# Kernel tuning notes

Hardware: AMD Instinct MI355X
Metric: run time of the kernel (lower is better)

The kernel has to match this reference:

```python
import jax, jax.numpy as jnp
import numpy as np

LAM = 1e-05
NUM_POINTS = 300
THRESHOLD = 0.5


def _sobel(img):
    # img: [B, 1, H, W] -> edge magnitude [B, 1, H, W]
    kx = jnp.array([[-1., 0., 1.], [-2., 0., 2.], [-1., 0., 1.]], jnp.float32).reshape(1, 1, 3, 3)
    ky = jnp.array([[-1., -2., -1.], [0., 0., 0.], [1., 2., 1.]], jnp.float32).reshape(1, 1, 3, 3)
    dn = jax.lax.conv_dimension_numbers(img.shape, kx.shape, ('NCHW', 'OIHW', 'NCHW'))
    ex = jax.lax.conv_general_dilated(img, kx, (1, 1), ((1, 1), (1, 1)), dimension_numbers=dn)
    ey = jax.lax.conv_general_dilated(img, ky, (1, 1), ((1, 1), (1, 1)), dimension_numbers=dn)
    return jnp.sqrt(ex ** 2 + ey ** 2)


def _select_points(edge_map, key):
    # JIT-friendly analogue of nonzero + randperm[:300]: random scores on
    # above-threshold pixels, take top NUM_POINTS; invalid slots are padded
    # with a duplicate of the first valid point (zero-length MST edges, so
    # they contribute nothing to total persistence, matching fewer points).
    H, W = edge_map.shape
    flat = edge_map.reshape(-1)
    mask = flat > THRESHOLD
    scores = jnp.where(mask, jax.random.uniform(key, flat.shape), -jnp.inf)
    _, idx = jax.lax.top_k(scores, NUM_POINTS)
    valid = mask[idx]
    pts = jnp.stack([idx // W, idx % W], axis=-1).astype(jnp.float32)  # (row, col)
    pts = jnp.where(valid[:, None], pts, pts[0])
    return pts


def _mst_total_persistence(pts):
    # H0 persistence of a Vietoris-Rips complex: births are 0, deaths are the
    # MST edge lengths (Prim's algorithm via lax.scan over N-1 steps).
    # total_persistence with exponent q=2: sum(death^2).
    d2 = jnp.sum((pts[:, None, :] - pts[None, :, :]) ** 2, axis=-1)
    D = jnp.sqrt(jnp.maximum(d2, 0.0))  # [N, N]
    n = pts.shape[0]
    in_tree = jnp.zeros((n,), dtype=bool).at[0].set(True)

    def step(carry, _):
        in_tree, mind = carry
        m = jnp.where(in_tree, jnp.inf, mind)
        j = jnp.argmin(m)
        w = m[j]
        in_tree = in_tree.at[j].set(True)
        mind = jnp.minimum(mind, D[j])
        return (in_tree, mind), w

    _, deaths = jax.lax.scan(step, (in_tree, D[0]), None, length=n - 1)
    return jnp.sum(deaths ** 2)


def _topo_loss(model_output, labels):
    pred_edges = _sobel(jax.nn.sigmoid(model_output))[:, 0]  # [B, H, W]
    mask_edges = _sobel(labels)[:, 0]                         # [B, H, W]
    B = pred_edges.shape[0]
    keys = jax.random.split(jax.random.key(42), 2 * B).reshape(B, 2)

    def per_sample(pe, me, k):
        pts_p = _select_points(pe, k[0])
        pts_m = _select_points(me, k[1])
        tp_p = _mst_total_persistence(pts_p)
        tp_m = _mst_total_persistence(pts_m)
        # SummaryStatisticLoss(total_persistence): |stat(mask) - stat(pred)|
        return jnp.abs(tp_m - tp_p)

    losses = jax.vmap(per_sample)(pred_edges, mask_edges, keys)
    return LAM * jnp.sum(losses) / B


def setup_inputs() -> dict:
    key = jax.random.key(0)
    k1, k2 = jax.random.split(key)
    model_output = jax.random.normal(k1, (32, 1, 512, 512), dtype=jnp.float32)
    labels = jax.random.uniform(k2, (32, 1, 512, 512), dtype=jnp.float32)
    return {"model_output": model_output, "labels": labels}


def reference(model_output, labels):
    return _topo_loss(model_output, labels)
```

## Files before the change

kernel.cpp:

```cpp
#include <hip/hip_runtime.h>
#include <cstdint>
#include <cstddef>

#define NPIX (512 * 512)
#define NMAPS 64
#define NPTS 300
#define CAP 2048
#define SLOTS 64
#define LBUFSZ 256
#define NWORDS 4096
#define TARGET 700.0
#define MT_BITS 0xFF63C000u

__device__ __forceinline__ uint32_t umin32(uint32_t a, uint32_t b) {
  return a < b ? a : b;
}

__device__ __forceinline__ void tf2x32(uint32_t k0, uint32_t k1,
                                       uint32_t x0, uint32_t x1,
                                       uint32_t& o0, uint32_t& o1) {
  uint32_t ks2 = k0 ^ k1 ^ 0x1BD11BDAu;
#define TFR(r) { x0 += x1; x1 = (x1 << (r)) | (x1 >> (32 - (r))); x1 ^= x0; }
  x0 += k0; x1 += k1;
  TFR(13) TFR(15) TFR(26) TFR(6)
  x0 += k1; x1 += ks2 + 1u;
  TFR(17) TFR(29) TFR(16) TFR(24)
  x0 += ks2; x1 += k0 + 2u;
  TFR(13) TFR(15) TFR(26) TFR(6)
  x0 += k0; x1 += k1 + 3u;
  TFR(17) TFR(29) TFR(16) TFR(24)
  x0 += k1; x1 += ks2 + 4u;
  TFR(13) TFR(15) TFR(26) TFR(6)
  x0 += ks2; x1 += k0 + 5u;
#undef TFR
  o0 = x0; o1 = x1;
}

__device__ __forceinline__ uint32_t score23(uint32_t k0, uint32_t k1, uint32_t p) {
  uint32_t a, b;
  tf2x32(k0, k1, 0u, p, a, b);
  return (a ^ b) >> 9;
}

__device__ __forceinline__ void map_key(int m, uint32_t& k0, uint32_t& k1) {
  tf2x32(0u, 42u, 0u, (uint32_t)m, k0, k1);
}

template <int CTRL>
__device__ __forceinline__ uint32_t dpp_mov_u32(uint32_t x) {
  return (uint32_t)__builtin_amdgcn_update_dpp((int)x, (int)x, CTRL, 0xF, 0xF,
                                               false);
}

__device__ __forceinline__ uint32_t wave_min_u32_bcast(uint32_t v) {
  v = umin32(v, dpp_mov_u32<0x111>(v));
  v = umin32(v, dpp_mov_u32<0x112>(v));
  v = umin32(v, dpp_mov_u32<0x114>(v));
  v = umin32(v, dpp_mov_u32<0x118>(v));
  v = umin32(v, dpp_mov_u32<0x142>(v));
  v = umin32(v, dpp_mov_u32<0x143>(v));
  return (uint32_t)__builtin_amdgcn_readlane((int)v, 63);
}

template <bool PRED, bool YIN>
__device__ __forceinline__ void edge_body(
    const float* __restrict__ src, unsigned long long* __restrict__ bitmap,
    unsigned int* __restrict__ wcnts, unsigned long long* lbuf,
    unsigned int* lcnt, int m, int l, int cs, int seg, int wi, uint32_t k0,
    uint32_t k1) {
  const int y0 = seg * 32;
  const int X = cs * 64 + l;
  const int hcol = (l == 0) ? X - 1 : ((l == 63) ? X + 1 : -1);
  const bool hok = (unsigned)hcol < 512u;

  auto val = [&](float t) -> float {
    if constexpr (PRED) return 1.f / (1.f + __expf(-t));
    else return t;
  };
  auto ldm = [&](int row) -> float {
    if constexpr (!YIN) {
      if ((unsigned)row >= 512u) return 0.f;
    }
    return val(src[row * 512 + X]);
  };
  auto ldh = [&](int row) -> float {
    if (!hok) return 0.f;
    if constexpr (!YIN) {
      if ((unsigned)row >= 512u) return 0.f;
    }
    return val(src[row * 512 + hcol]);
  };

  float a = ldm(y0 - 1), b = ldm(y0);
  float ha = ldh(y0 - 1), hb = ldh(y0);
  unsigned int cnt = 0;

  for (int i = 0; i < 32; ++i) {
    const int y = y0 + i;
    float c = ldm(y + 1), hc = ldh(y + 1);

    float t = a + 2.f * b + c;
    float u = c - a;
    float th = ha + 2.f * hb + hc;
    float uh = hc - ha;

    float tL = __shfl_up(t, 1);   if (l == 0)  tL = th;
    float tR = __shfl_down(t, 1); if (l == 63) tR = th;
    float uL = __shfl_up(u, 1);   if (l == 0)  uL = uh;
    float uR = __shfl_down(u, 1); if (l == 63) uR = uh;

    float ex = tR - tL;
    float ey = uL + 2.f * u + uR;
    bool bit = (ex * ex + ey * ey) > 0.25f;

    unsigned long long ball = __ballot(bit);
    if (l == 0) {
      bitmap[(size_t)m * NWORDS + (size_t)y * 8 + cs] = ball;
      cnt += (unsigned int)__popcll(ball);
    }
    if (bit) {
      uint32_t p = (uint32_t)(y * 512 + X);
      uint32_t o0, o1;
      tf2x32(k0, k1, 0u, p, o0, o1);
      uint32_t x = o0 ^ o1;
      if (x >= MT_BITS) {
        unsigned int pos = atomicAdd(lcnt, 1u);
        if (pos < LBUFSZ)
          lbuf[pos] = ((unsigned long long)(x >> 9) << 32) | (uint32_t)(~p);
      }
    }
    a = b; b = c; ha = hb; hb = hc;
  }
  if (l == 0) wcnts[m * 128 + wi] = cnt;
}

__global__ __launch_bounds__(256) void edge_collect_kernel(
    const float* __restrict__ mo, const float* __restrict__ lb,
    unsigned long long* __restrict__ bitmap, unsigned int* __restrict__ wcnts,
    unsigned long long* __restrict__ cand, unsigned int* __restrict__ bcnt,
    float* __restrict__ out) {
  const int m = blockIdx.y;
  const int which = m & 1;
  const int bx = blockIdx.x;
  const float* __restrict__ src = (which ? lb : mo) + (size_t)(m >> 1) * NPIX;
  const int l = threadIdx.x & 63;
  const int wi = bx * 4 + (threadIdx.x >> 6);
  const int cs = wi & 7;
  const int seg = wi >> 3;

  if (m == 0 && bx == 0 && threadIdx.x == 0) out[0] = 0.f;

  __shared__ unsigned long long lbuf[LBUFSZ];
  __shared__ unsigned int lcnt;
  if (threadIdx.x == 0) lcnt = 0;
  __syncthreads();

  uint32_t k0, k1;
  map_key(m, k0, k1);

  const bool yin = (seg != 0) && (seg != 15);
  if (which) {
    if (yin) edge_body<false, true>(src, bitmap, wcnts, lbuf, &lcnt, m, l, cs, seg, wi, k0, k1);
    else     edge_body<false, false>(src, bitmap, wcnts, lbuf, &lcnt, m, l, cs, seg, wi, k0, k1);
  } else {
    if (yin) edge_body<true, true>(src, bitmap, wcnts, lbuf, &lcnt, m, l, cs, seg, wi, k0, k1);
    else     edge_body<true, false>(src, bitmap, wcnts, lbuf, &lcnt, m, l, cs, seg, wi, k0, k1);
  }

  __syncthreads();
  const unsigned int total = lcnt;
  const unsigned int cc = total < SLOTS ? total : SLOTS;
  for (unsigned int i = threadIdx.x; i < cc; i += 256)
    cand[(size_t)m * CAP + bx * SLOTS + i] = lbuf[i];
  if (threadIdx.x == 0) bcnt[m * 32 + bx] = total;
}

__device__ __forceinline__ void reduce_N(const unsigned int* __restrict__ wcnts,
                                         int m, int tid, unsigned int* sN) {
  if (tid < 64) {
    unsigned int v = wcnts[m * 128 + tid] + wcnts[m * 128 + 64 + tid];
#pragma unroll
    for (int off = 32; off > 0; off >>= 1) v += __shfl_xor(v, off, 64);
    if (tid == 0) *sN = v;
  }
}

__global__ __launch_bounds__(256) void select_kernel(
    const unsigned long long* __restrict__ bitmap,
    const unsigned int* __restrict__ wcnts,
    const unsigned long long* __restrict__ cand,
    const unsigned int* __restrict__ bcnt,
    uint32_t* __restrict__ pts, unsigned int* __restrict__ nsel) {
  const int m = blockIdx.x;
  const int tid = threadIdx.x;
  __shared__ unsigned long long buf[CAP];
  __shared__ unsigned int hist[256];
  __shared__ unsigned int scnt32[32];
  __shared__ unsigned int sbase[33];
  __shared__ unsigned int s_tot, s_cnt, s_b, s_rank, sN, s_ovf;

  reduce_N(wcnts, m, tid, &sN);
  if (tid < 32) scnt32[tid] = bcnt[m * 32 + tid];
  __syncthreads();
  const unsigned int N = sN;
  if (N == 0) { if (tid == 0) nsel[m] = 0; return; }
  const unsigned int need = N < NPTS ? N : NPTS;

  if (tid == 0) {
    unsigned int s = 0, ovf = 0;
    for (int i = 0; i < 32; ++i) {
      sbase[i] = s;
      unsigned int cg = scnt32[i];
      if (cg > SLOTS) ovf = 1;
      s += cg < SLOTS ? cg : SLOTS;
    }
    sbase[32] = s;
    s_ovf = ovf;
  }
  __syncthreads();

  unsigned int c;
  if (!s_ovf && sbase[32] >= need) {
    c = sbase[32];
    const int g = tid >> 3, j0 = tid & 7;
    const unsigned int cg = scnt32[g] < SLOTS ? scnt32[g] : SLOTS;
    for (unsigned int i = j0; i < cg; i += 8)
      buf[sbase[g] + i] = cand[(size_t)m * CAP + g * SLOTS + i];
    __syncthreads();
  } else {
    uint32_t k0, k1;
    map_key(m, k0, k1);
    const unsigned long long* __restrict__ wmap = bitmap + (size_t)m * NWORDS;
    unsigned int mt = 0, cnt = 0;
    double target = TARGET;
    for (int iter = 0; iter < 16; ++iter) {
      mt = ((double)N > target)
               ? (unsigned int)(8388608.0 * (1.0 - target / (double)N))
               : 0u;
      if (tid == 0) s_tot = 0;
      __syncthreads();
      unsigned int lc = 0;
      for (int w = tid; w < NWORDS; w += 256) {
        unsigned long long word = wmap[w];
        while (word) {
          int bpos = __builtin_ctzll(word);
          word &= word - 1;
          uint32_t p = ((uint32_t)w << 6) + (uint32_t)bpos;
          lc += (score23(k0, k1, p) >= mt) ? 1u : 0u;
        }
      }
      if (lc) atomicAdd(&s_tot, lc);
      __syncthreads();
      cnt = s_tot;
      __syncthreads();
      if (cnt >= need && cnt <= CAP) break;
      if (cnt < need) target *= 3.0; else target *= 0.5;
    }
    if (tid == 0) s_cnt = 0;
    __syncthreads();
    for (int w = tid; w < NWORDS; w += 256) {
      unsigned long long word = wmap[w];
      while (word) {
        int bpos = __builtin_ctzll(word);
        word &= word - 1;
        uint32_t p = ((uint32_t)w << 6) + (uint32_t)bpos;
        uint32_t sc = score23(k0, k1, p);
        if (sc >= mt) {
          unsigned int pos = atomicAdd(&s_cnt, 1u);
          if (pos < CAP)
            buf[pos] = ((unsigned long long)sc << 32) | (uint32_t)(~p);
        }
      }
    }
    __syncthreads();
    c = s_cnt < CAP ? s_cnt : CAP;
    __syncthreads();
  }

  unsigned long long T = 0ull;
  if (c > need) {
    unsigned int rank = need;
    unsigned long long prefix = 0ull;
    for (int sh = 48; sh >= 0; sh -= 8) {
      hist[tid] = 0;
      __syncthreads();
      for (unsigned int i = tid; i < c; i += 256) {
        unsigned long long k = buf[i];
        if ((k >> (sh + 8)) == (prefix >> (sh + 8)))
          atomicAdd(&hist[(unsigned int)(k >> sh) & 255u], 1u);
      }
      __syncthreads();
      if (tid < 64) {
        unsigned int h0 = hist[4 * tid], h1 = hist[4 * tid + 1];
        unsigned int h2 = hist[4 * tid + 2], h3 = hist[4 * tid + 3];
        unsigned int gsum = h0 + h1 + h2 + h3;
        unsigned int s = gsum;
#pragma unroll
        for (int off = 1; off < 64; off <<= 1) {
          unsigned int o = __shfl_down(s, off, 64);
          s += (tid + off < 64) ? o : 0u;
        }
        unsigned int above = s - gsum;
        unsigned int S3 = above, S2 = S3 + h3, S1 = S2 + h2, S0 = S1 + h1;
        if (S3 < rank && rank <= S3 + h3) { s_b = 4 * tid + 3; s_rank = rank - S3; }
        if (S2 < rank && rank <= S2 + h2) { s_b = 4 * tid + 2; s_rank = rank - S2; }
        if (S1 < rank && rank <= S1 + h1) { s_b = 4 * tid + 1; s_rank = rank - S1; }
        if (S0 < rank && rank <= S0 + h0) { s_b = 4 * tid + 0; s_rank = rank - S0; }
      }
      __syncthreads();
      prefix |= ((unsigned long long)s_b) << sh;
      rank = s_rank;
    }
    T = prefix;
  }

  if (tid == 0) s_cnt = 0;
  __syncthreads();
  for (unsigned int i = tid; i < c; i += 256) {
    unsigned long long k = buf[i];
    if (k >= T) {
      unsigned int pos = atomicAdd(&s_cnt, 1u);
      if (pos < NPTS) {
        uint32_t p = ~(uint32_t)k;
        pts[(size_t)m * NPTS + pos] = ((p >> 9) << 16) | (p & 511u);
      }
    }
  }
  __syncthreads();
  if (tid == 0) nsel[m] = s_cnt < need ? s_cnt : need;
}

__global__ __launch_bounds__(128, 1) void mst_kernel(
    const uint32_t* __restrict__ pts, const unsigned int* __restrict__ nsel,
    float* __restrict__ out) {
  const int wv = threadIdx.x >> 6;
  const int m = blockIdx.x * 2 + wv;
  const int l = threadIdx.x & 63;
  const int n = (int)nsel[m];
  __shared__ float stp[2];

  unsigned int utp = 0;
  if (n > 1) {
    uint32_t pk[5], key[5];
    int px[5], py[5];
#pragma unroll
    for (int k = 0; k < 5; ++k) {
      int id = k * 64 + l;
      pk[k] = (id < n) ? pts[(size_t)m * NPTS + id] : 0u;
    }
    const uint32_t p0 = (uint32_t)__builtin_amdgcn_readlane((int)pk[0], 0);
    const int x0 = (int)(p0 >> 16), y0 = (int)(p0 & 0xFFFFu);
#pragma unroll
    for (int k = 0; k < 5; ++k) {
      int id = k * 64 + l;
      px[k] = (int)(pk[k] >> 16);
      py[k] = (int)(pk[k] & 0xFFFFu);
      if (id > 0 && id < n) {
        int dx = px[k] - x0, dy = py[k] - y0;
        key[k] = ((uint32_t)(__mul24(dx, dx) + __mul24(dy, dy)) << 9) |
                 (uint32_t)id;
      } else {
        key[k] = 0xFFFFFFFFu;
      }
    }

    for (int it = 0; it < n - 1; ++it) {
      uint32_t best = umin32(umin32(umin32(key[0], key[1]),
                                    umin32(key[2], key[3])), key[4]);
      best = wave_min_u32_bcast(best);
      utp += best >> 9;
      const int j = (int)(best & 511u);
      const int ko = j >> 6, lo = j & 63;
      uint32_t cp = pk[0];
#pragma unroll
      for (int k = 1; k < 5; ++k) cp = (ko == k) ? pk[k] : cp;
      const uint32_t pj = (uint32_t)__builtin_amdgcn_readlane((int)cp, lo);
      const int jx = (int)(pj >> 16), jy = (int)(pj & 0xFFFFu);
#pragma unroll
      for (int k = 0; k < 5; ++k) {
        int dx = px[k] - jx, dy = py[k] - jy;
        uint32_t nk = ((uint32_t)(__mul24(dx, dx) + __mul24(dy, dy)) << 9) |
                      (uint32_t)(k * 64 + l);
        uint32_t upd =
            (key[k] == 0xFFFFFFFFu) ? 0xFFFFFFFFu : umin32(key[k], nk);
        key[k] = (k == ko && l == lo) ? 0xFFFFFFFFu : upd;
      }
    }
  }
  if (l == 0) stp[wv] = (float)utp;
  __syncthreads();
  if (threadIdx.x == 0)
    atomicAdd(out, 1e-5f * fabsf(stp[1] - stp[0]) / 32.f);
}

extern "C" void kernel_launch(void* const* d_in, const int* in_sizes, int n_in,
                              void* d_out, int out_size, void* d_ws,
                              size_t ws_size, hipStream_t stream) {
  const float* mo = (const float*)d_in[0];
  const float* lb = (const float*)d_in[1];
  float* out = (float*)d_out;
  char* ws = (char*)d_ws;

  unsigned long long* bitmap = (unsigned long long*)ws;
  unsigned long long* cand = (unsigned long long*)(ws + 2097152);
  unsigned int* wcnts = (unsigned int*)(ws + 3145728);
  unsigned int* bcnt  = (unsigned int*)(ws + 3178496);
  unsigned int* nsel  = (unsigned int*)(ws + 3186688);
  uint32_t* pts       = (uint32_t*)(ws + 3186944);

  edge_collect_kernel<<<dim3(32, 64), 256, 0, stream>>>(mo, lb, bitmap, wcnts,
                                                        cand, bcnt, out);
  select_kernel<<<NMAPS, 256, 0, stream>>>(bitmap, wcnts, cand, bcnt, pts,
                                           nsel);
  mst_kernel<<<32, 128, 0, stream>>>(pts, nsel, out);
}
```

Before: 239.0 us.

## Vectorize Sobel edge pass to float4 per lane with 8-row strips

Each lane now processes four adjacent columns using float4 loads, and each wave covers a 256-column half-row over 8 rows instead of a 64-column strip over 32 rows. Bitmap words are assembled from per-lane nibbles with DPP OR reductions, and the next row is prefetched. The random key is made wave-uniform with readfirstlane. This aims to cut load instruction count and shuffle overhead, and to raise memory-level parallelism in the bandwidth-bound edge pass. In exchange it adds more halo reloads per row strip and extra DPP work.

Result: faster. 226.8 us (-5.1%).

```diff
diff --git a/kernel.cpp b/kernel.cpp
--- a/kernel.cpp
+++ b/kernel.cpp
@@ -52,6 +52,12 @@
                                                false);
 }
 
+template <int CTRL>
+__device__ __forceinline__ uint32_t dpp_or0(uint32_t x) {
+  return (uint32_t)__builtin_amdgcn_update_dpp(0, (int)x, CTRL, 0xF, 0xF,
+                                               false);
+}
+
 __device__ __forceinline__ uint32_t wave_min_u32_bcast(uint32_t v) {
   v = umin32(v, dpp_mov_u32<0x111>(v));
   v = umin32(v, dpp_mov_u32<0x112>(v));
@@ -63,75 +69,125 @@
 }
 
 template <bool PRED, bool YIN>
+__device__ __forceinline__ float4 ld4row(const float* __restrict__ src,
+                                         int row, int X0) {
+  if constexpr (!YIN) {
+    if ((unsigned)row >= 512u) return make_float4(0.f, 0.f, 0.f, 0.f);
+  }
+  float4 v = *reinterpret_cast<const float4*>(src + (size_t)row * 512 + X0);
+  if constexpr (PRED) {
+    v.x = 1.f / (1.f + __expf(-v.x));
+    v.y = 1.f / (1.f + __expf(-v.y));
+    v.z = 1.f / (1.f + __expf(-v.z));
+    v.w = 1.f / (1.f + __expf(-v.w));
+  }
+  return v;
+}
+
+template <bool PRED, bool YIN>
+__device__ __forceinline__ float ldhrow(const float* __restrict__ src,
+                                        int row, int hx, bool hact) {
+  if (!hact) return 0.f;
+  if constexpr (!YIN) {
+    if ((unsigned)row >= 512u) return 0.f;
+  }
+  float t = src[(size_t)row * 512 + hx];
+  if constexpr (PRED) t = 1.f / (1.f + __expf(-t));
+  return t;
+}
+
+__device__ __forceinline__ void push_surv(unsigned long long* lbuf,
+                                          unsigned int* lcnt, uint32_t x,
+                                          uint32_t p) {
+  unsigned int pos = atomicAdd(lcnt, 1u);
+  if (pos < LBUFSZ)
+    lbuf[pos] = ((unsigned long long)(x >> 9) << 32) | (uint32_t)(~p);
+}
+
+template <bool PRED, bool YIN>
 __device__ __forceinline__ void edge_body(
     const float* __restrict__ src, unsigned long long* __restrict__ bitmap,
     unsigned int* __restrict__ wcnts, unsigned long long* lbuf,
-    unsigned int* lcnt, int m, int l, int cs, int seg, int wi, uint32_t k0,
+    unsigned int* lcnt, int m, int l, int h, int r, int wi, uint32_t k0,
     uint32_t k1) {
-  const int y0 = seg * 32;
-  const int X = cs * 64 + l;
-  const int hcol = (l == 0) ? X - 1 : ((l == 63) ? X + 1 : -1);
-  const bool hok = (unsigned)hcol < 512u;
-
-  auto val = [&](float t) -> float {
-    if constexpr (PRED) return 1.f / (1.f + __expf(-t));
-    else return t;
-  };
-  auto ldm = [&](int row) -> float {
-    if constexpr (!YIN) {
-      if ((unsigned)row >= 512u) return 0.f;
-    }
-    return val(src[row * 512 + X]);
-  };
-  auto ldh = [&](int row) -> float {
-    if (!hok) return 0.f;
-    if constexpr (!YIN) {
-      if ((unsigned)row >= 512u) return 0.f;
-    }
-    return val(src[row * 512 + hcol]);
-  };
-
-  float a = ldm(y0 - 1), b = ldm(y0);
-  float ha = ldh(y0 - 1), hb = ldh(y0);
+  const int y0 = r * 8;
+  const int X0 = h * 256 + l * 4;
+  const int hx = 256 - h;
+  const bool hact = h ? (l == 0) : (l == 63);
+  const int lr = l & 15;
+
+  float4 a = ld4row<PRED, YIN>(src, y0 - 1, X0);
+  float4 b = ld4row<PRED, YIN>(src, y0, X0);
+  float ha = ldhrow<PRED, YIN>(src, y0 - 1, hx, hact);
+  float hb = ldhrow<PRED, YIN>(src, y0, hx, hact);
+  float4 cn = ld4row<PRED, YIN>(src, y0 + 1, X0);
+  float hcn = ldhrow<PRED, YIN>(src, y0 + 1, hx, hact);
+
   unsigned int cnt = 0;
-
-  for (int i = 0; i < 32; ++i) {
+  unsigned long long* __restrict__ bm =
+      bitmap + (size_t)m * NWORDS + (h * 4 + (l >> 4));
+
+#pragma unroll 2
+  for (int i = 0; i < 8; ++i) {
     const int y = y0 + i;
-    float c = ldm(y + 1), hc = ldh(y + 1);
-
-    float t = a + 2.f * b + c;
-    float u = c - a;
-    float th = ha + 2.f * hb + hc;
-    float uh = hc - ha;
-
-    float tL = __shfl_up(t, 1);   if (l == 0)  tL = th;
-    float tR = __shfl_down(t, 1); if (l == 63) tR = th;
-    float uL = __shfl_up(u, 1);   if (l == 0)  uL = uh;
-    float uR = __shfl_down(u, 1); if (l == 63) uR = uh;
-
-    float ex = tR - tL;
-    float ey = uL + 2.f * u + uR;
-    bool bit = (ex * ex + ey * ey) > 0.25f;
-
-    unsigned long long ball = __ballot(bit);
-    if (l == 0) {
-      bitmap[(size_t)m * NWORDS + (size_t)y * 8 + cs] = ball;
-      cnt += (unsigned int)__popcll(ball);
-    }
-    if (bit) {
-      uint32_t p = (uint32_t)(y * 512 + X);
-      uint32_t o0, o1;
-      tf2x32(k0, k1, 0u, p, o0, o1);
-      uint32_t x = o0 ^ o1;
-      if (x >= MT_BITS) {
-        unsigned int pos = atomicAdd(lcnt, 1u);
-        if (pos < LBUFSZ)
-          lbuf[pos] = ((unsigned long long)(x >> 9) << 32) | (uint32_t)(~p);
-      }
-    }
+    float4 c = cn;
+    float hc = hcn;
+    if (i < 7) {
+      cn = ld4row<PRED, YIN>(src, y + 2, X0);
+      hcn = ldhrow<PRED, YIN>(src, y + 2, hx, hact);
+    }
+
+    float t0 = a.x + 2.f * b.x + c.x, t1 = a.y + 2.f * b.y + c.y;
+    float t2 = a.z + 2.f * b.z + c.z, t3 = a.w + 2.f * b.w + c.w;
+    float u0 = c.x - a.x, u1 = c.y - a.y, u2 = c.z - a.z, u3 = c.w - a.w;
+    float th = ha + 2.f * hb + hc, uh = hc - ha;
+
+    float tU = __shfl_up(t3, 1), uU = __shfl_up(u3, 1);
+    float tD = __shfl_down(t0, 1), uD = __shfl_down(u0, 1);
+    if (l == 0) { tU = th; uU = uh; }
+    if (l == 63) { tD = th; uD = uh; }
+
+    float ex0 = t1 - tU, ex1 = t2 - t0, ex2 = t3 - t1, ex3 = tD - t2;
+    float ey0 = uU + 2.f * u0 + u1, ey1 = u0 + 2.f * u1 + u2;
+    float ey2 = u1 + 2.f * u2 + u3, ey3 = u2 + 2.f * u3 + uD;
+
+    bool b0 = ex0 * ex0 + ey0 * ey0 > 0.25f;
+    bool b1 = ex1 * ex1 + ey1 * ey1 > 0.25f;
+    bool b2 = ex2 * ex2 + ey2 * ey2 > 0.25f;
+    bool b3 = ex3 * ex3 + ey3 * ey3 > 0.25f;
+
+    const uint32_t pb = (uint32_t)(y * 512 + X0);
+    uint32_t q0, q1, q2, q3;
+    { uint32_t o0, o1; tf2x32(k0, k1, 0u, pb + 0u, o0, o1); q0 = o0 ^ o1; }
+    { uint32_t o0, o1; tf2x32(k0, k1, 0u, pb + 1u, o0, o1); q1 = o0 ^ o1; }
+    { uint32_t o0, o1; tf2x32(k0, k1, 0u, pb + 2u, o0, o1); q2 = o0 ^ o1; }
+    { uint32_t o0, o1; tf2x32(k0, k1, 0u, pb + 3u, o0, o1); q3 = o0 ^ o1; }
+
+    if (b0 && q0 >= MT_BITS) push_surv(lbuf, lcnt, q0, pb + 0u);
+    if (b1 && q1 >= MT_BITS) push_surv(lbuf, lcnt, q1, pb + 1u);
+    if (b2 && q2 >= MT_BITS) push_surv(lbuf, lcnt, q2, pb + 2u);
+    if (b3 && q3 >= MT_BITS) push_surv(lbuf, lcnt, q3, pb + 3u);
+
+    uint32_t nib = (b0 ? 1u : 0u) | (b1 ? 2u : 0u) | (b2 ? 4u : 0u) |
+                   (b3 ? 8u : 0u);
+    unsigned long long full = (unsigned long long)nib << (4 * lr);
+    uint32_t wlo = (uint32_t)full, whi = (uint32_t)(full >> 32);
+    wlo |= dpp_or0<0x111>(wlo); whi |= dpp_or0<0x111>(whi);
+    wlo |= dpp_or0<0x112>(wlo); whi |= dpp_or0<0x112>(whi);
+    wlo |= dpp_or0<0x114>(wlo); whi |= dpp_or0<0x114>(whi);
+    wlo |= dpp_or0<0x118>(wlo); whi |= dpp_or0<0x118>(whi);
+    if (lr == 15) {
+      unsigned long long word = ((unsigned long long)whi << 32) | wlo;
+      bm[(size_t)y * 8] = word;
+      cnt += (unsigned int)__popcll(word);
+    }
+
     a = b; b = c; ha = hb; hb = hc;
   }
-  if (l == 0) wcnts[m * 128 + wi] = cnt;
+
+  cnt += __shfl_xor(cnt, 16);
+  cnt += __shfl_xor(cnt, 32);
+  if (l == 15) wcnts[m * 128 + wi] = cnt;
 }
 
 __global__ __launch_bounds__(256) void edge_collect_kernel(
@@ -145,8 +201,8 @@
   const float* __restrict__ src = (which ? lb : mo) + (size_t)(m >> 1) * NPIX;
   const int l = threadIdx.x & 63;
   const int wi = bx * 4 + (threadIdx.x >> 6);
-  const int cs = wi & 7;
-  const int seg = wi >> 3;
+  const int h = wi & 1;
+  const int r = wi >> 1;
 
   if (m == 0 && bx == 0 && threadIdx.x == 0) out[0] = 0.f;
 
@@ -157,14 +213,16 @@
 
   uint32_t k0, k1;
   map_key(m, k0, k1);
-
-  const bool yin = (seg != 0) && (seg != 15);
+  k0 = (uint32_t)__builtin_amdgcn_readfirstlane((int)k0);
+  k1 = (uint32_t)__builtin_amdgcn_readfirstlane((int)k1);
+
+  const bool yin = (r != 0) && (r != 63);
   if (which) {
-    if (yin) edge_body<false, true>(src, bitmap, wcnts, lbuf, &lcnt, m, l, cs, seg, wi, k0, k1);
-    else     edge_body<false, false>(src, bitmap, wcnts, lbuf, &lcnt, m, l, cs, seg, wi, k0, k1);
+    if (yin) edge_body<false, true>(src, bitmap, wcnts, lbuf, &lcnt, m, l, h, r, wi, k0, k1);
+    else     edge_body<false, false>(src, bitmap, wcnts, lbuf, &lcnt, m, l, h, r, wi, k0, k1);
   } else {
-    if (yin) edge_body<true, true>(src, bitmap, wcnts, lbuf, &lcnt, m, l, cs, seg, wi, k0, k1);
-    else     edge_body<true, false>(src, bitmap, wcnts, lbuf, &lcnt, m, l, cs, seg, wi, k0, k1);
+    if (yin) edge_body<true, true>(src, bitmap, wcnts, lbuf, &lcnt, m, l, h, r, wi, k0, k1);
+    else     edge_body<true, false>(src, bitmap, wcnts, lbuf, &lcnt, m, l, h, r, wi, k0, k1);
   }
 
   __syncthreads();
```
